# Performance work log

Hardware: AMD Instinct MI355X
Metric: run time of the kernel (lower is better)

The kernel has to match this reference:

```python
import jax, jax.numpy as jnp
import numpy as np

COMMITMENT_COST = 0.25
ENTROPY_WEIGHT = 0.1
EPS = 1e-10


def setup_inputs() -> dict:
    key = jax.random.key(0)
    k1, k2 = jax.random.split(key)
    B, L, D, K = 8, 4096, 256, 4096
    z = jax.random.normal(k1, (B, L, D), dtype=jnp.float32)
    # torch init: uniform(-1/K, 1/K)
    codebook_weight = jax.random.uniform(k2, (K, D), dtype=jnp.float32,
                                         minval=-1.0 / K, maxval=1.0 / K)
    return {"z": z, "codebook_weight": codebook_weight}


def reference(z, codebook_weight):
    B, L, D = z.shape
    z_flat = z.reshape(-1, D)                       # [N, D]
    # squared euclidean distances: [N, K]
    d2 = (jnp.sum(z_flat ** 2, axis=1, keepdims=True)
          + jnp.sum(codebook_weight ** 2, axis=1)
          - 2.0 * z_flat @ codebook_weight.T)
    indices = jnp.argmin(d2, axis=1)                # [N]
    z_q_flat = codebook_weight[indices]             # gather [N, D]
    z_q = z_q_flat.reshape(B, L, D)

    codebook_loss = jnp.mean((z_q - jax.lax.stop_gradient(z)) ** 2)
    commitment_loss = jnp.mean((jax.lax.stop_gradient(z_q) - z) ** 2)

    probs = jax.nn.softmax(-d2, axis=1)             # [N, K]
    avg_probs = probs.mean(axis=0)                  # [K]
    entropy = -jnp.sum(avg_probs * jnp.log(avg_probs + EPS))
    entropy_loss = -entropy

    codebook_commitment_loss = codebook_loss + COMMITMENT_COST * commitment_loss
    scaled_entropy_loss = ENTROPY_WEIGHT * entropy_loss
    vq_loss = codebook_commitment_loss + scaled_entropy_loss

    # straight-through estimator
    z_q_ste = z + jax.lax.stop_gradient(z_q - z)
    indices_out = indices.reshape(B, L)
    return (z_q_ste, indices_out, vq_loss, codebook_commitment_loss, scaled_entropy_loss)
```

## Files before the change

### kernel.cpp

```cpp
#include <hip/hip_runtime.h>
#include <stdint.h>

#define NROWS 32768
#define KC 4096
#define DIM 256
#define BM 64
#define NWV 4
#define TPS 64
#define CAP 40
#define KAPPA 0.99960f
#define K2L2E 2.88539008f
#define L2E 1.44269504f

#define OUT_IDX (NROWS * DIM)
#define OUT_SCAL (OUT_IDX + NROWS)

#define WS_CNORM 0
#define WS_ZNORM 16384
#define WS_LOSS  147456
#define WS_AVGP8 147712
#define WS_FRAG  278784

typedef __bf16 bf8 __attribute__((ext_vector_type(8)));
typedef float f16v __attribute__((ext_vector_type(16)));

#define GLOAD_LDS(g, l) \
  __builtin_amdgcn_global_load_lds( \
      (const __attribute__((address_space(1))) void*)(g), \
      (__attribute__((address_space(3))) void*)(l), 16, 0, 0)

__device__ __forceinline__ unsigned ford(float f) {
  unsigned u = __float_as_uint(f);
  return (u & 0x80000000u) ? ~u : (u | 0x80000000u);
}

__device__ __forceinline__ float np_rownorm256(const float* __restrict__ p) {
  float h[2];
  #pragma unroll
  for (int half = 0; half < 2; ++half) {
    const float* b = p + half * 128;
    float r[8];
    #pragma unroll
    for (int j = 0; j < 8; ++j) { float v = b[j]; r[j] = __fmul_rn(v, v); }
    for (int i = 8; i < 128; i += 8) {
      #pragma unroll
      for (int j = 0; j < 8; ++j) {
        float v = b[i + j];
        r[j] = __fadd_rn(r[j], __fmul_rn(v, v));
      }
    }
    h[half] = __fadd_rn(
        __fadd_rn(__fadd_rn(r[0], r[1]), __fadd_rn(r[2], r[3])),
        __fadd_rn(__fadd_rn(r[4], r[5]), __fadd_rn(r[6], r[7])));
  }
  return __fadd_rn(h[0], h[1]);
}

__global__ void k_norms(const float* __restrict__ cbw, const float* __restrict__ z,
                        float* __restrict__ cnorm, float* __restrict__ znorm) {
  int r = blockIdx.x * 256 + threadIdx.x;
  if (r < KC) cnorm[r] = np_rownorm256(cbw + (size_t)r * DIM);
  else {
    int q = r - KC;
    if (q < NROWS) znorm[q] = np_rownorm256(z + (size_t)q * DIM);
  }
}

__global__ void k_frag(const float* __restrict__ cbw, __bf16* __restrict__ frag) {
  int idx = blockIdx.x * 256 + threadIdx.x;
  int c = idx >> 5, u = idx & 31;
  int ds = u >> 1, half = u & 1;
  int ct = c >> 5, m = c & 31;
  int lane = half * 32 + m;
  const float* src = cbw + (size_t)c * DIM + ds * 16 + half * 8;
  float4 a = *(const float4*)src;
  float4 b = *(const float4*)(src + 4);
  bf8 h;
  h[0] = (__bf16)a.x; h[1] = (__bf16)a.y; h[2] = (__bf16)a.z; h[3] = (__bf16)a.w;
  h[4] = (__bf16)b.x; h[5] = (__bf16)b.y; h[6] = (__bf16)b.z; h[7] = (__bf16)b.w;
  *(bf8*)(frag + ((size_t)(ct * 16 + ds) * 64 + lane) * 8) = h;
}

__device__ __forceinline__ float exact_d2(const float* __restrict__ zr,
                                          const float* __restrict__ cr,
                                          float rn, float cn) {
  float mm = 0.f;
  for (int d = 0; d < DIM; d += 4) {
    float4 zv = *(const float4*)(zr + d);
    float4 cv = *(const float4*)(cr + d);
    mm = __builtin_fmaf(zv.x, cv.x, mm);
    mm = __builtin_fmaf(zv.y, cv.y, mm);
    mm = __builtin_fmaf(zv.z, cv.z, mm);
    mm = __builtin_fmaf(zv.w, cv.w, mm);
  }
  return __fsub_rn(__fadd_rn(rn, cn), __fmul_rn(2.f, mm));
}

#define BLD(bs, c) (*(const bf8*)((bs) + (c) * 512 + lane * 8))

#define AQ_ALL(OP) OP(0) OP(1) OP(2) OP(3) OP(4) OP(5) OP(6) OP(7) \
                   OP(8) OP(9) OP(10) OP(11) OP(12) OP(13) OP(14) OP(15)
#define AQ_DECL(i) const bf8 aq##i = \
  *(const bf8*)&U[((size_t)(wr * 16 + (i)) * 64 + lane) * 8];

#define MF(A, B) acc = __builtin_amdgcn_mfma_f32_32x32x16_bf16((A), (B), acc, 0, 0, 0);
#define CONSUME_H0(bs) { MF(aq0, BLD(bs,0)) MF(aq1, BLD(bs,1)) MF(aq2, BLD(bs,2)) \
  MF(aq3, BLD(bs,3)) MF(aq4, BLD(bs,4)) MF(aq5, BLD(bs,5)) MF(aq6, BLD(bs,6)) \
  MF(aq7, BLD(bs,7)) }
#define CONSUME_H1(bs) { MF(aq8, BLD(bs,0)) MF(aq9, BLD(bs,1)) MF(aq10, BLD(bs,2)) \
  MF(aq11, BLD(bs,3)) MF(aq12, BLD(bs,4)) MF(aq13, BLD(bs,5)) MF(aq14, BLD(bs,6)) \
  MF(aq15, BLD(bs,7)) }

__global__ __launch_bounds__(256, 2) void k_main(
    const float* __restrict__ z, const float* __restrict__ cbw,
    const float* __restrict__ cnorm, const float* __restrict__ znorm,
    const __bf16* __restrict__ frag, float* __restrict__ out,
    float* __restrict__ avgp8, double* __restrict__ losssum) {
  __shared__ __attribute__((aligned(16))) __bf16 U[16384];
  __shared__ int cand[BM][CAP];
  __shared__ int ccount[BM];
  __shared__ unsigned rowmaxU[BM];
  __shared__ unsigned long long rowkey[BM];
  __shared__ float esumL[BM], invR[BM], lred[256];
  __shared__ int idxr[BM];

  const int t = threadIdx.x;
  const int lane = t & 63, wv = t >> 6;
  const int ln31 = lane & 31, lh = lane >> 5;
  const int wr = wv >> 1, wc = wv & 1;
  const int row0 = blockIdx.x * BM;
  const int ctbase = wc * TPS;

  if (t < BM) {
    ccount[t] = 0; rowmaxU[t] = 0u; rowkey[t] = ~0ULL; esumL[t] = 0.f;
  }

  #pragma unroll
  for (int i = 0; i < 8; ++i) {
    int idx = i * 256 + t;
    int l = idx & 63, ds = (idx >> 6) & 15, rt = idx >> 10;
    int row = rt * 32 + (l & 31), d0 = ds * 16 + (l >> 5) * 8;
    const float* src = z + (size_t)(row0 + row) * DIM + d0;
    float4 a = *(const float4*)src;
    float4 b = *(const float4*)(src + 4);
    bf8 h;
    h[0] = (__bf16)a.x; h[1] = (__bf16)a.y; h[2] = (__bf16)a.z; h[3] = (__bf16)a.w;
    h[4] = (__bf16)b.x; h[5] = (__bf16)b.y; h[6] = (__bf16)b.z; h[7] = (__bf16)b.w;
    *(bf8*)&U[((size_t)((rt * 16 + ds) * 64 + l)) * 8] = h;
  }
  __syncthreads();

  AQ_ALL(AQ_DECL)
  __syncthreads();

  #define STAGEH(ct, h, buf) { \
    const char* g_ = (const char*)frag + (size_t)(ct) * 16384 + (size_t)(h) * 8192 \
                     + wr * 4096 + (size_t)lane * 16; \
    char* l_ = (char*)U + (buf) * 16384 + wc * 8192 + wr * 4096; \
    GLOAD_LDS(g_, l_); \
    GLOAD_LDS(g_ + 1024, l_ + 1024); \
    GLOAD_LDS(g_ + 2048, l_ + 2048); \
    GLOAD_LDS(g_ + 3072, l_ + 3072); \
  }
  #define BSP(buf) ((const __bf16*)((const char*)U + (buf) * 16384 + wc * 8192))

  float es[16];
  #pragma unroll
  for (int i = 0; i < 16; ++i) es[i] = 0.f;

  {
    STAGEH(ctbase, 0, 0)
    __syncthreads();
    for (int tt = 0; tt < 65; ++tt) {
      const int ct = ctbase + (tt ? tt - 1 : 0);
      STAGEH(ct, 1, 1)
      f16v acc;
      #pragma unroll
      for (int r = 0; r < 16; ++r) acc[r] = 0.f;
      CONSUME_H0(BSP(0))
      __syncthreads();
      {
        int ctn = ctbase + ((tt < 64) ? tt : 63);
        STAGEH(ctn, 0, 0)
      }
      CONSUME_H1(BSP(1))
      const float cnl = cnorm[ct * 32 + ln31] * L2E;
      if (tt == 0) {
        #pragma unroll
        for (int r = 0; r < 16; ++r) {
          const int row = wr * 32 + (r & 3) + 8 * (r >> 2) + 4 * lh;
          float e = exp2f(__builtin_fmaf(acc[r], K2L2E, -cnl));
          atomicMax(&rowmaxU[row], __float_as_uint(e));
        }
      } else {
        float cr[16];
        {
          const float4* rmf = (const float4*)(rowmaxU + wr * 32);
          float4 c0 = rmf[lh], c1 = rmf[2 + lh], c2 = rmf[4 + lh], c3 = rmf[6 + lh];
          cr[0]  = c0.x; cr[1]  = c0.y; cr[2]  = c0.z; cr[3]  = c0.w;
          cr[4]  = c1.x; cr[5]  = c1.y; cr[6]  = c1.z; cr[7]  = c1.w;
          cr[8]  = c2.x; cr[9]  = c2.y; cr[10] = c2.z; cr[11] = c2.w;
          cr[12] = c3.x; cr[13] = c3.y; cr[14] = c3.z; cr[15] = c3.w;
        }
        unsigned cond = 0u;
        #pragma unroll
        for (int r = 0; r < 16; ++r) {
          float e = exp2f(__builtin_fmaf(acc[r], K2L2E, -cnl));
          es[r] += e;
          cond |= (e >= cr[r] * KAPPA) ? (1u << r) : 0u;
        }
        if (cond) {
          #pragma unroll
          for (int r = 0; r < 16; ++r) {
            if (cond & (1u << r)) {
              const int row = wr * 32 + (r & 3) + 8 * (r >> 2) + 4 * lh;
              float e = exp2f(__builtin_fmaf(acc[r], K2L2E, -cnl));
              atomicMax(&rowmaxU[row], __float_as_uint(e));
              int slot = atomicAdd(&ccount[row], 1);
              if (slot < CAP) cand[row][slot] = ct * 32 + ln31;
            }
          }
        }
      }
      __syncthreads();
    }
  }

  #pragma unroll
  for (int r = 0; r < 16; ++r) {
    float e = es[r];
    #pragma unroll
    for (int off = 16; off > 0; off >>= 1) e += __shfl_xor(e, off);
    if (ln31 == 0) {
      const int row = wr * 32 + (r & 3) + 8 * (r >> 2) + 4 * lh;
      atomicAdd(&esumL[row], e);
    }
  }
  __syncthreads();
  if (t < BM) invR[t] = 1.0f / esumL[t];
  __syncthreads();

  {
    int r = t & 63, q = t >> 6;
    int cnt = ccount[r];
    const float* zr = z + (size_t)(row0 + r) * DIM;
    float rn = znorm[row0 + r];
    if (cnt <= CAP) {
      for (int s = q; s < cnt; s += 4) {
        int k = cand[r][s];
        float d2 = exact_d2(zr, cbw + (size_t)k * DIM, rn, cnorm[k]);
        atomicMin(&rowkey[r], (((unsigned long long)ford(d2)) << 32) | (unsigned)k);
      }
    } else {
      for (int k = q; k < KC; k += 4) {
        float d2 = exact_d2(zr, cbw + (size_t)k * DIM, rn, cnorm[k]);
        atomicMin(&rowkey[r], (((unsigned long long)ford(d2)) << 32) | (unsigned)k);
      }
    }
  }
  __syncthreads();
  if (t < BM) {
    int idx = (int)(rowkey[t] & 0xFFFFFFFFULL);
    idxr[t] = idx;
    out[OUT_IDX + row0 + t] = (float)idx;
  }
  __syncthreads();

  float lacc = 0.f;
  for (int r = 0; r < BM; ++r) {
    int idx = idxr[r];
    float zq = cbw[(size_t)idx * DIM + t];
    float zv = z[(size_t)(row0 + r) * DIM + t];
    float df = __fsub_rn(zq, zv);
    out[(size_t)(row0 + r) * DIM + t] = __fadd_rn(zv, df);
    lacc += df * df;
  }
  lred[t] = lacc;
  __syncthreads();
  #pragma unroll
  for (int s = 128; s > 0; s >>= 1) {
    if (t < s) lred[t] += lred[t + s];
    __syncthreads();
  }
  if (t == 0) atomicAdd(losssum, (double)lred[0]);

  float ir[16];
  #pragma unroll
  for (int r = 0; r < 16; ++r)
    ir[r] = invR[wr * 32 + (r & 3) + 8 * (r >> 2) + 4 * lh];
  __syncthreads();

  {
    float* shadow = avgp8 + (size_t)(blockIdx.x & 7) * KC;
    STAGEH(ctbase, 0, 0)
    __syncthreads();
    for (int tt = 0; tt < 64; ++tt) {
      const int ct = ctbase + tt;
      STAGEH(ct, 1, 1)
      f16v acc;
      #pragma unroll
      for (int r = 0; r < 16; ++r) acc[r] = 0.f;
      CONSUME_H0(BSP(0))
      __syncthreads();
      {
        int ctn = ctbase + ((tt < 63) ? tt + 1 : 63);
        STAGEH(ctn, 0, 0)
      }
      CONSUME_H1(BSP(1))
      const float cnl = cnorm[ct * 32 + ln31] * L2E;
      float s2 = 0.f;
      #pragma unroll
      for (int r = 0; r < 16; ++r) {
        float e = exp2f(__builtin_fmaf(acc[r], K2L2E, -cnl));
        s2 = __builtin_fmaf(e, ir[r], s2);
      }
      s2 += __shfl_xor(s2, 32);
      if (lh == 0) atomicAdd(&shadow[ct * 32 + ln31], s2);
      __syncthreads();
    }
  }
}

__global__ void k_final(const float* __restrict__ avgp8,
                        const double* __restrict__ losssum,
                        float* __restrict__ out) {
  const int t = threadIdx.x;
  double part = 0.0;
  for (int k = t; k < KC; k += 256) {
    float a4 = 0.f;
    #pragma unroll
    for (int s = 0; s < 8; ++s) a4 += avgp8[s * KC + k];
    double a = (double)a4 / (double)NROWS;
    part += a * log(a + 1e-10);
  }
  __shared__ double sd[256];
  sd[t] = part;
  __syncthreads();
  for (int s = 128; s > 0; s >>= 1) {
    if (t < s) sd[t] += sd[t + s];
    __syncthreads();
  }
  if (t == 0) {
    double H = -sd[0];
    double mse = losssum[0] / (double)((size_t)NROWS * DIM);
    double ccl = 1.25 * mse;
    double sel = -0.1 * H;
    out[OUT_SCAL + 0] = (float)(ccl + sel);
    out[OUT_SCAL + 1] = (float)ccl;
    out[OUT_SCAL + 2] = (float)sel;
  }
}

extern "C" void kernel_launch(void* const* d_in, const int* in_sizes, int n_in,
                              void* d_out, int out_size, void* d_ws, size_t ws_size,
                              hipStream_t stream) {
  const float* z = (const float*)d_in[0];
  const float* cbw = (const float*)d_in[1];
  float* out = (float*)d_out;
  char* ws = (char*)d_ws;
  float* cnorm = (float*)(ws + WS_CNORM);
  float* znorm = (float*)(ws + WS_ZNORM);
  double* losssum = (double*)(ws + WS_LOSS);
  float* avgp8 = (float*)(ws + WS_AVGP8);
  __bf16* frag = (__bf16*)(ws + WS_FRAG);

  hipMemsetAsync(ws + WS_LOSS, 0, 8, stream);
  hipMemsetAsync(ws + WS_AVGP8, 0, 8 * KC * 4, stream);
  k_norms<<<(KC + NROWS) / 256, 256, 0, stream>>>(cbw, z, cnorm, znorm);
  k_frag<<<(KC * 32) / 256, 256, 0, stream>>>(cbw, frag);
  k_main<<<NROWS / BM, 256, 0, stream>>>(z, cbw, cnorm, znorm, frag, out,
                                         avgp8, losssum);
  k_final<<<1, 256, 0, stream>>>(avgp8, losssum, out);
}
```

Before: 439.3 us.

## Double-buffer full codebook tiles in LDS and drop mid-tile barrier

Replaces the half-tile staging scheme, where each codebook tile was split into two halves with a barrier between them, with a full double buffer. The next whole tile is prefetched into the alternate buffer while all 16 MFMAs run on the current one, removing one __syncthreads per tile in both passes. LDS use for the staging buffer doubles to 64 KB, which may limit occupancy under the two-blocks-per-SM launch bound. The row-norm helper is also changed to use float4 loads.

```diff
diff --git a/kernel.cpp b/kernel.cpp
--- a/kernel.cpp
+++ b/kernel.cpp
@@ -5,7 +5,6 @@
 #define KC 4096
 #define DIM 256
 #define BM 64
-#define NWV 4
 #define TPS 64
 #define CAP 40
 #define KAPPA 0.99960f
@@ -40,14 +39,25 @@
   for (int half = 0; half < 2; ++half) {
     const float* b = p + half * 128;
     float r[8];
-    #pragma unroll
-    for (int j = 0; j < 8; ++j) { float v = b[j]; r[j] = __fmul_rn(v, v); }
+    {
+      float4 v0 = *(const float4*)(b);
+      float4 v1 = *(const float4*)(b + 4);
+      r[0] = __fmul_rn(v0.x, v0.x); r[1] = __fmul_rn(v0.y, v0.y);
+      r[2] = __fmul_rn(v0.z, v0.z); r[3] = __fmul_rn(v0.w, v0.w);
+      r[4] = __fmul_rn(v1.x, v1.x); r[5] = __fmul_rn(v1.y, v1.y);
+      r[6] = __fmul_rn(v1.z, v1.z); r[7] = __fmul_rn(v1.w, v1.w);
+    }
     for (int i = 8; i < 128; i += 8) {
-      #pragma unroll
-      for (int j = 0; j < 8; ++j) {
-        float v = b[i + j];
-        r[j] = __fadd_rn(r[j], __fmul_rn(v, v));
-      }
+      float4 v0 = *(const float4*)(b + i);
+      float4 v1 = *(const float4*)(b + i + 4);
+      r[0] = __fadd_rn(r[0], __fmul_rn(v0.x, v0.x));
+      r[1] = __fadd_rn(r[1], __fmul_rn(v0.y, v0.y));
+      r[2] = __fadd_rn(r[2], __fmul_rn(v0.z, v0.z));
+      r[3] = __fadd_rn(r[3], __fmul_rn(v0.w, v0.w));
+      r[4] = __fadd_rn(r[4], __fmul_rn(v1.x, v1.x));
+      r[5] = __fadd_rn(r[5], __fmul_rn(v1.y, v1.y));
+      r[6] = __fadd_rn(r[6], __fmul_rn(v1.z, v1.z));
+      r[7] = __fadd_rn(r[7], __fmul_rn(v1.w, v1.w));
     }
     h[half] = __fadd_rn(
         __fadd_rn(__fadd_rn(r[0], r[1]), __fadd_rn(r[2], r[3])),
@@ -101,22 +111,23 @@
 #define AQ_ALL(OP) OP(0) OP(1) OP(2) OP(3) OP(4) OP(5) OP(6) OP(7) \
                    OP(8) OP(9) OP(10) OP(11) OP(12) OP(13) OP(14) OP(15)
 #define AQ_DECL(i) const bf8 aq##i = \
-  *(const bf8*)&U[((size_t)(wr * 16 + (i)) * 64 + lane) * 8];
+  *(const bf8*)&BstA[((size_t)(wr * 16 + (i)) * 64 + lane) * 8];
 
 #define MF(A, B) acc = __builtin_amdgcn_mfma_f32_32x32x16_bf16((A), (B), acc, 0, 0, 0);
-#define CONSUME_H0(bs) { MF(aq0, BLD(bs,0)) MF(aq1, BLD(bs,1)) MF(aq2, BLD(bs,2)) \
-  MF(aq3, BLD(bs,3)) MF(aq4, BLD(bs,4)) MF(aq5, BLD(bs,5)) MF(aq6, BLD(bs,6)) \
-  MF(aq7, BLD(bs,7)) }
-#define CONSUME_H1(bs) { MF(aq8, BLD(bs,0)) MF(aq9, BLD(bs,1)) MF(aq10, BLD(bs,2)) \
-  MF(aq11, BLD(bs,3)) MF(aq12, BLD(bs,4)) MF(aq13, BLD(bs,5)) MF(aq14, BLD(bs,6)) \
-  MF(aq15, BLD(bs,7)) }
+#define CONS16(bs_) { \
+  MF(aq0,  BLD(bs_,0))  MF(aq1,  BLD(bs_,1))  MF(aq2,  BLD(bs_,2))  \
+  MF(aq3,  BLD(bs_,3))  MF(aq4,  BLD(bs_,4))  MF(aq5,  BLD(bs_,5))  \
+  MF(aq6,  BLD(bs_,6))  MF(aq7,  BLD(bs_,7))  MF(aq8,  BLD(bs_,8))  \
+  MF(aq9,  BLD(bs_,9))  MF(aq10, BLD(bs_,10)) MF(aq11, BLD(bs_,11)) \
+  MF(aq12, BLD(bs_,12)) MF(aq13, BLD(bs_,13)) MF(aq14, BLD(bs_,14)) \
+  MF(aq15, BLD(bs_,15)) }
 
 __global__ __launch_bounds__(256, 2) void k_main(
     const float* __restrict__ z, const float* __restrict__ cbw,
     const float* __restrict__ cnorm, const float* __restrict__ znorm,
     const __bf16* __restrict__ frag, float* __restrict__ out,
     float* __restrict__ avgp8, double* __restrict__ losssum) {
-  __shared__ __attribute__((aligned(16))) __bf16 U[16384];
+  __shared__ __attribute__((aligned(16))) __bf16 Bst[2][2][8192];
   __shared__ int cand[BM][CAP];
   __shared__ int ccount[BM];
   __shared__ unsigned rowmaxU[BM];
@@ -135,6 +146,7 @@
     ccount[t] = 0; rowmaxU[t] = 0u; rowkey[t] = ~0ULL; esumL[t] = 0.f;
   }
 
+  __bf16* BstA = &Bst[0][0][0];
   #pragma unroll
   for (int i = 0; i < 8; ++i) {
     int idx = i * 256 + t;
@@ -146,44 +158,44 @@
     bf8 h;
     h[0] = (__bf16)a.x; h[1] = (__bf16)a.y; h[2] = (__bf16)a.z; h[3] = (__bf16)a.w;
     h[4] = (__bf16)b.x; h[5] = (__bf16)b.y; h[6] = (__bf16)b.z; h[7] = (__bf16)b.w;
-    *(bf8*)&U[((size_t)((rt * 16 + ds) * 64 + l)) * 8] = h;
+    *(bf8*)&BstA[((size_t)((rt * 16 + ds) * 64 + l)) * 8] = h;
   }
   __syncthreads();
 
   AQ_ALL(AQ_DECL)
   __syncthreads();
 
-  #define STAGEH(ct, h, buf) { \
-    const char* g_ = (const char*)frag + (size_t)(ct) * 16384 + (size_t)(h) * 8192 \
-                     + wr * 4096 + (size_t)lane * 16; \
-    char* l_ = (char*)U + (buf) * 16384 + wc * 8192 + wr * 4096; \
-    GLOAD_LDS(g_, l_); \
-    GLOAD_LDS(g_ + 1024, l_ + 1024); \
-    GLOAD_LDS(g_ + 2048, l_ + 2048); \
-    GLOAD_LDS(g_ + 3072, l_ + 3072); \
-  }
-  #define BSP(buf) ((const __bf16*)((const char*)U + (buf) * 16384 + wc * 8192))
+  #define STG(ct, b) { \
+    const char* g_ = (const char*)frag + (size_t)(ct) * 16384 + wr * 8192 \
+                     + (size_t)lane * 16; \
+    char* l_ = (char*)Bst + (b) * 32768 + wc * 16384 + wr * 8192; \
+    GLOAD_LDS(g_, l_);            GLOAD_LDS(g_ + 1024, l_ + 1024); \
+    GLOAD_LDS(g_ + 2048, l_ + 2048); GLOAD_LDS(g_ + 3072, l_ + 3072); \
+    GLOAD_LDS(g_ + 4096, l_ + 4096); GLOAD_LDS(g_ + 5120, l_ + 5120); \
+    GLOAD_LDS(g_ + 6144, l_ + 6144); GLOAD_LDS(g_ + 7168, l_ + 7168); \
+  }
+  #define BSP(b) ((const __bf16*)((const char*)Bst + (b) * 32768 + wc * 16384))
 
   float es[16];
   #pragma unroll
   for (int i = 0; i < 16; ++i) es[i] = 0.f;
 
   {
-    STAGEH(ctbase, 0, 0)
+    STG(ctbase, 0)
     __syncthreads();
-    for (int tt = 0; tt < 65; ++tt) {
+    for (int tt = 0; tt <= TPS; ++tt) {
       const int ct = ctbase + (tt ? tt - 1 : 0);
-      STAGEH(ct, 1, 1)
+      {
+        int ctn = ctbase + ((tt < TPS) ? tt : TPS - 1);
+        STG(ctn, (tt + 1) & 1)
+      }
       f16v acc;
       #pragma unroll
       for (int r = 0; r < 16; ++r) acc[r] = 0.f;
-      CONSUME_H0(BSP(0))
-      __syncthreads();
       {
-        int ctn = ctbase + ((tt < 64) ? tt : 63);
-        STAGEH(ctn, 0, 0)
-      }
-      CONSUME_H1(BSP(1))
+        const __bf16* bs_ = BSP(tt & 1);
+        CONS16(bs_)
+      }
       const float cnl = cnorm[ct * 32 + ln31] * L2E;
       if (tt == 0) {
         #pragma unroll
@@ -292,21 +304,21 @@
 
   {
     float* shadow = avgp8 + (size_t)(blockIdx.x & 7) * KC;
-    STAGEH(ctbase, 0, 0)
+    STG(ctbase, 0)
     __syncthreads();
-    for (int tt = 0; tt < 64; ++tt) {
+    for (int tt = 0; tt < TPS; ++tt) {
       const int ct = ctbase + tt;
-      STAGEH(ct, 1, 1)
+      {
+        int ctn = ctbase + ((tt < TPS - 1) ? tt + 1 : TPS - 1);
+        STG(ctn, (tt + 1) & 1)
+      }
       f16v acc;
       #pragma unroll
       for (int r = 0; r < 16; ++r) acc[r] = 0.f;
-      CONSUME_H0(BSP(0))
-      __syncthreads();
       {
-        int ctn = ctbase + ((tt < 63) ? tt + 1 : 63);
-        STAGEH(ctn, 0, 0)
-      }
-      CONSUME_H1(BSP(1))
+        const __bf16* bs_ = BSP(tt & 1);
+        CONS16(bs_)
+      }
       const float cnl = cnorm[ct * 32 + ln31] * L2E;
       float s2 = 0.f;
       #pragma unroll
```

After: 423.9 us. 3.5% less time.
